# Performance work log

Measured on AMD Instinct MI355X. Metric: run time of the kernel, lower is better.

Reference implementation:

```python
import jax, jax.numpy as jnp
import numpy as np
from jax import lax

D_MODEL = 1024
EXPAND = 2
D_INNER = EXPAND * D_MODEL  # 2048
D_STATE = 16
D_CONV = 4
DT_RANK = -(-D_INNER // 16)  # ceil(d_inner/16) = 128
BATCH, SEQLEN = 2, 1024
LN_EPS = 1e-5


def setup_inputs() -> dict:
    key = jax.random.key(0)
    ks = jax.random.split(key, 8)
    s = lambda n: 1.0 / np.sqrt(n)
    x = jax.random.normal(ks[0], (BATCH, SEQLEN, D_MODEL), jnp.float32)
    ln_gamma = jnp.ones((D_MODEL,), jnp.float32)
    ln_beta = jnp.zeros((D_MODEL,), jnp.float32)
    in_proj_w = jax.random.normal(ks[1], (D_MODEL, 2 * D_INNER), jnp.float32) * s(D_MODEL)
    conv_w = jax.random.normal(ks[2], (D_INNER, D_CONV), jnp.float32) * s(D_CONV)
    conv_b = jnp.zeros((D_INNER,), jnp.float32)
    x_proj_w = jax.random.normal(ks[3], (D_INNER, DT_RANK + 2 * D_STATE), jnp.float32) * s(D_INNER)
    dt_proj_w = jax.random.uniform(ks[4], (DT_RANK, D_INNER), jnp.float32,
                                   -DT_RANK ** -0.5, DT_RANK ** -0.5)
    # dt bias init: inverse-softplus of dt ~ LogUniform(1e-3, 1e-1)
    dt = jnp.exp(jax.random.uniform(ks[5], (D_INNER,), jnp.float32)
                 * (np.log(0.1) - np.log(0.001)) + np.log(0.001))
    dt = jnp.clip(dt, 1e-4)
    dt_proj_b = dt + jnp.log(-jnp.expm1(-dt))
    A_log = jnp.log(jnp.tile(jnp.arange(1, D_STATE + 1, dtype=jnp.float32)[None, :],
                             (D_INNER, 1)))  # (D_INNER, D_STATE)
    D_param = jnp.ones((D_INNER,), jnp.float32)
    out_proj_w = jax.random.normal(ks[6], (D_INNER, D_MODEL), jnp.float32) * s(D_INNER)
    return {"x": x, "ln_gamma": ln_gamma, "ln_beta": ln_beta, "in_proj_w": in_proj_w,
            "conv_w": conv_w, "conv_b": conv_b, "x_proj_w": x_proj_w,
            "dt_proj_w": dt_proj_w, "dt_proj_b": dt_proj_b, "A_log": A_log,
            "D_param": D_param, "out_proj_w": out_proj_w}


def _layernorm(x, gamma, beta):
    mu = jnp.mean(x, -1, keepdims=True)
    var = jnp.mean(jnp.square(x - mu), -1, keepdims=True)
    return (x - mu) * lax.rsqrt(var + LN_EPS) * gamma + beta


def reference(x, ln_gamma, ln_beta, in_proj_w, conv_w, conv_b, x_proj_w,
              dt_proj_w, dt_proj_b, A_log, D_param, out_proj_w):
    B, L, _ = x.shape
    residual = x
    h = _layernorm(x, ln_gamma, ln_beta)
    xz = h @ in_proj_w                               # (B, L, 2*Di)
    xb, z = jnp.split(xz, 2, axis=-1)                # each (B, L, Di)

    # Depthwise causal conv1d (left pad d_conv-1, truncate to L)
    xp = jnp.pad(xb, ((0, 0), (D_CONV - 1, 0), (0, 0)))
    xc = sum(xp[:, k:k + L, :] * conv_w[:, k] for k in range(D_CONV)) + conv_b
    xb = jax.nn.silu(xc)                             # (B, L, Di)

    # Selective SSM
    xpj = xb @ x_proj_w                              # (B, L, dt_rank + 2N)
    dt_r = xpj[..., :DT_RANK]
    B_mat = xpj[..., DT_RANK:DT_RANK + D_STATE]      # (B, L, N)
    C_mat = xpj[..., DT_RANK + D_STATE:]             # (B, L, N)
    delta = jax.nn.softplus(dt_r @ dt_proj_w + dt_proj_b)  # (B, L, Di)
    A = -jnp.exp(A_log)                              # (Di, N)
    dA = jnp.exp(delta[..., None] * A)               # (B, L, Di, N)
    dBx = delta[..., None] * B_mat[:, :, None, :] * xb[..., None]  # (B, L, Di, N)

    def step(hcar, inp):
        dA_t, dBx_t, C_t = inp                       # (B,Di,N),(B,Di,N),(B,N)
        hcar = dA_t * hcar + dBx_t
        y_t = jnp.einsum('bdn,bn->bd', hcar, C_t)
        return hcar, y_t

    h0 = jnp.zeros((B, D_INNER, D_STATE), xb.dtype)
    _, ys = lax.scan(step, h0, (dA.transpose(1, 0, 2, 3),
                                dBx.transpose(1, 0, 2, 3),
                                C_mat.transpose(1, 0, 2)))
    y = ys.transpose(1, 0, 2) + xb * D_param         # (B, L, Di)

    y = y * jax.nn.silu(z)
    return y @ out_proj_w + residual
```

## Files before the change

### kernel.cpp

```cpp
#include <hip/hip_runtime.h>
#include <hip/hip_bf16.h>

#define D_MODEL 1024
#define D_INNER 2048
#define NPROJ   4096
#define D_STATE 16
#define DT_RANK 128
#define XPJ_N   160
#define SEQLEN  1024
#define BATCH   2
#define NTOK    2048
#define CHUNK   16
#define NCHUNK  (SEQLEN / CHUNK)
#define LOG2_NCHUNK 6
#define SPLITK  8
#define OP_SPLITK 4

typedef short short8 __attribute__((ext_vector_type(8)));
typedef unsigned short ushort8v __attribute__((ext_vector_type(8)));
typedef float f32x4 __attribute__((ext_vector_type(4)));

__device__ __forceinline__ float sigmoidf_(float x) { return 1.f / (1.f + __expf(-x)); }
__device__ __forceinline__ ushort f2bf_bits(float f) {
    __hip_bfloat16 h = __float2bfloat16(f);
    return *(ushort*)&h;
}
__device__ __forceinline__ float bf2f(ushort u) {
    union { unsigned int i; float f; } v;
    v.i = ((unsigned int)u) << 16;
    return v.f;
}
#define LOG2E 1.44269504088896f

__device__ __forceinline__ void transpose_tile(const float* __restrict__ in,
                                               ushort* __restrict__ out,
                                               int R, int C, int cx, int ry)
{
    __shared__ float tile[64][65];
    int c0 = cx * 64, r0 = ry * 64;
    #pragma unroll
    for (int i = 0; i < 16; ++i) {
        int idx = threadIdx.x + i * 256;
        int r = idx >> 6, c = idx & 63;
        tile[r][c] = (r0 + r < R && c0 + c < C) ? in[(long)(r0 + r) * C + (c0 + c)] : 0.f;
    }
    __syncthreads();
    #pragma unroll
    for (int i = 0; i < 16; ++i) {
        int idx = threadIdx.x + i * 256;
        int cc = idx >> 6, rr = idx & 63;
        if (c0 + cc < C && r0 + rr < R)
            out[(long)(c0 + cc) * R + (r0 + rr)] = f2bf_bits(tile[rr][cc]);
    }
}

__device__ __forceinline__ void ln_row(const float* __restrict__ x,
                                       const float* __restrict__ g,
                                       const float* __restrict__ be,
                                       ushort* __restrict__ hb, int row)
{
    __shared__ float red[8];
    const float4* xr = (const float4*)(x + (long)row * D_MODEL);
    float4 v = xr[threadIdx.x];
    float s1 = v.x + v.y + v.z + v.w;
    float s2 = v.x*v.x + v.y*v.y + v.z*v.z + v.w*v.w;
    for (int off = 32; off >= 1; off >>= 1) {
        s1 += __shfl_down(s1, off);
        s2 += __shfl_down(s2, off);
    }
    int wid = threadIdx.x >> 6;
    if ((threadIdx.x & 63) == 0) { red[wid] = s1; red[4 + wid] = s2; }
    __syncthreads();
    float mu  = (red[0] + red[1] + red[2] + red[3]) * (1.f / D_MODEL);
    float ex2 = (red[4] + red[5] + red[6] + red[7]) * (1.f / D_MODEL);
    float inv = rsqrtf(ex2 - mu * mu + 1e-5f);
    float4 g4 = ((const float4*)g)[threadIdx.x];
    float4 b4 = ((const float4*)be)[threadIdx.x];
    ushort4 o;
    o.x = f2bf_bits((v.x - mu) * inv * g4.x + b4.x);
    o.y = f2bf_bits((v.y - mu) * inv * g4.y + b4.y);
    o.z = f2bf_bits((v.z - mu) * inv * g4.z + b4.z);
    o.w = f2bf_bits((v.w - mu) * inv * g4.w + b4.w);
    *(ushort4*)(hb + (long)row * D_MODEL + threadIdx.x * 4) = o;
}

__global__ __launch_bounds__(256) void prep_kernel(const float* __restrict__ w2,
                                                   ushort* __restrict__ W2T,
                                                   const float* __restrict__ w7,
                                                   ushort* __restrict__ W7T,
                                                   const float* __restrict__ xp,
                                                   ushort* __restrict__ XPT,
                                                   const float* __restrict__ dt,
                                                   ushort* __restrict__ DTT,
                                                   const float* __restrict__ x,
                                                   const float* __restrict__ g,
                                                   const float* __restrict__ be,
                                                   ushort* __restrict__ hb)
{
    int idx = blockIdx.x;
    if (idx < 1024) {
        transpose_tile(w2, W2T, D_MODEL, NPROJ, idx & 63, idx >> 6);
    } else if (idx < 1536) {
        int rel = idx - 1024;
        transpose_tile(w7, W7T, D_INNER, D_MODEL, rel & 15, rel >> 4);
    } else if (idx < 1632) {
        int rel = idx - 1536;
        transpose_tile(xp, XPT, D_INNER, XPJ_N, rel % 3, rel / 3);
    } else if (idx < 1696) {
        int rel = idx - 1632;
        transpose_tile(dt, DTT, DT_RANK, D_INNER, rel & 31, rel >> 5);
    } else {
        ln_row(x, g, be, hb, idx - 1696);
    }
}

template <int EPI, int OBF>
__global__ __launch_bounds__(256) void gemm_mfma_kernel(const ushort* __restrict__ A,
                                                        const ushort* __restrict__ Bt,
                                                        const float* __restrict__ bias,
                                                        float* __restrict__ Cf,
                                                        ushort* __restrict__ Cb,
                                                        int M, int N, int K, int lda, int ldb)
{
    long zoff = (long)blockIdx.z;
    A  += zoff * K;
    Bt += zoff * K;
    if (OBF == 0) Cf += zoff * (long)M * N;
    else          Cb += zoff * (long)M * N;
    int lin = blockIdx.y * gridDim.x + blockIdx.x;
    int cpx = (gridDim.x * gridDim.y) >> 3;
    lin = (lin & 7) * cpx + (lin >> 3);
    int bx = lin % gridDim.x, by = lin / gridDim.x;
    __shared__ __align__(16) ushort Al[2][128 * 32];
    __shared__ __align__(16) ushort Bl[2][128 * 32];
    int tid = threadIdx.x;
    int lane = tid & 63;
    int w = tid >> 6, wr = w >> 1, wc = w & 1;
    int m0 = by * 128, n0 = bx * 128;
    f32x4 acc[4][4];
    #pragma unroll
    for (int m = 0; m < 4; ++m)
        #pragma unroll
        for (int n = 0; n < 4; ++n) acc[m][n] = (f32x4){0.f, 0.f, 0.f, 0.f};
    int l15 = lane & 15, kq = lane >> 4;

    auto stage = [&](int buf, int k0) {
        #pragma unroll
        for (int i = 0; i < 2; ++i) {
            int s = i * 256 + tid;
            int row = s >> 2, kg = s & 3;
            int kgl = kg ^ ((row >> 1) & 3);
            __builtin_amdgcn_global_load_lds(
                (const __attribute__((address_space(1))) void*)(A + (long)(m0 + row) * lda + k0 + kgl * 8),
                (__attribute__((address_space(3))) void*)(Al[buf] + s * 8), 16, 0, 0);
            __builtin_amdgcn_global_load_lds(
                (const __attribute__((address_space(1))) void*)(Bt + (long)(n0 + row) * ldb + k0 + kgl * 8),
                (__attribute__((address_space(3))) void*)(Bl[buf] + s * 8), 16, 0, 0);
        }
    };

    stage(0, 0);
    int cur = 0;
    for (int k0 = 0; k0 < K; k0 += 32) {
        if (k0 + 32 < K) {
            stage(cur ^ 1, k0 + 32);
            asm volatile("s_waitcnt vmcnt(4)" ::: "memory");
        } else {
            asm volatile("s_waitcnt vmcnt(0)" ::: "memory");
        }
        __builtin_amdgcn_s_barrier();
        asm volatile("" ::: "memory");
        short8 af[4], bf[4];
        #pragma unroll
        for (int m = 0; m < 4; ++m) {
            int row = wr * 64 + m * 16 + l15;
            af[m] = *(const short8*)&Al[cur][row * 32 + (kq ^ ((row >> 1) & 3)) * 8];
        }
        #pragma unroll
        for (int n = 0; n < 4; ++n) {
            int row = wc * 64 + n * 16 + l15;
            bf[n] = *(const short8*)&Bl[cur][row * 32 + (kq ^ ((row >> 1) & 3)) * 8];
        }
        __builtin_amdgcn_s_setprio(1);
        #pragma unroll
        for (int m = 0; m < 4; ++m)
            #pragma unroll
            for (int n = 0; n < 4; ++n)
                acc[m][n] = __builtin_amdgcn_mfma_f32_16x16x32_bf16(af[m], bf[n], acc[m][n], 0, 0, 0);
        __builtin_amdgcn_s_setprio(0);
        asm volatile("" ::: "memory");
        __builtin_amdgcn_s_barrier();
        asm volatile("" ::: "memory");
        cur ^= 1;
    }
    #pragma unroll
    for (int m = 0; m < 4; ++m) {
        #pragma unroll
        for (int n = 0; n < 4; ++n) {
            #pragma unroll
            for (int r = 0; r < 4; ++r) {
                int row = m0 + wr * 64 + m * 16 + kq * 4 + r;
                int col = n0 + wc * 64 + n * 16 + l15;
                float v = acc[m][n][r];
                if (EPI == 1) {
                    v += bias[col];
                    v = (v > 20.f) ? v : log1pf(__expf(v));
                }
                if (OBF) Cb[(long)row * N + col] = f2bf_bits(v);
                else     Cf[(long)row * N + col] = v;
            }
        }
    }
}

template <int EPI, int OBF>
__global__ __launch_bounds__(256) void gemm_mfma64_kernel(const ushort* __restrict__ A,
                                                          const ushort* __restrict__ Bt,
                                                          const float* __restrict__ bias,
                                                          float* __restrict__ Cf,
                                                          ushort* __restrict__ Cb,
                                                          int M, int N, int K)
{
    int lin = blockIdx.y * gridDim.x + blockIdx.x;
    int cpx = (gridDim.x * gridDim.y) >> 3;
    lin = (lin & 7) * cpx + (lin >> 3);
    int bx = lin % gridDim.x, by = lin / gridDim.x;
    __shared__ __align__(16) ushort Al[2][128 * 32];
    __shared__ __align__(16) ushort Bl[2][64 * 32];
    int tid = threadIdx.x;
    int lane = tid & 63;
    int w = tid >> 6, wr = w >> 1, wc = w & 1;
    int m0 = by * 128, n0 = bx * 64;
    f32x4 acc[4][2];
    #pragma unroll
    for (int m = 0; m < 4; ++m)
        #pragma unroll
        for (int n = 0; n < 2; ++n) acc[m][n] = (f32x4){0.f, 0.f, 0.f, 0.f};
    int l15 = lane & 15, kq = lane >> 4;

    auto stage = [&](int buf, int k0) {
        #pragma unroll
        for (int i = 0; i < 2; ++i) {
            int s = i * 256 + tid;
            int row = s >> 2, kg = s & 3;
            int kgl = kg ^ ((row >> 1) & 3);
            __builtin_amdgcn_global_load_lds(
                (const __attribute__((address_space(1))) void*)(A + (long)(m0 + row) * K + k0 + kgl * 8),
                (__attribute__((address_space(3))) void*)(Al[buf] + s * 8), 16, 0, 0);
        }
        {
            int s = tid;
            int row = s >> 2, kg = s & 3;
            int kgl = kg ^ ((row >> 1) & 3);
            __builtin_amdgcn_global_load_lds(
                (const __attribute__((address_space(1))) void*)(Bt + (long)(n0 + row) * K + k0 + kgl * 8),
                (__attribute__((address_space(3))) void*)(Bl[buf] + s * 8), 16, 0, 0);
        }
    };

    stage(0, 0);
    int cur = 0;
    for (int k0 = 0; k0 < K; k0 += 32) {
        if (k0 + 32 < K) {
            stage(cur ^ 1, k0 + 32);
            asm volatile("s_waitcnt vmcnt(3)" ::: "memory");
        } else {
            asm volatile("s_waitcnt vmcnt(0)" ::: "memory");
        }
        __builtin_amdgcn_s_barrier();
        asm volatile("" ::: "memory");
        short8 af[4], bf[2];
        #pragma unroll
        for (int m = 0; m < 4; ++m) {
            int row = wr * 64 + m * 16 + l15;
            af[m] = *(const short8*)&Al[cur][row * 32 + (kq ^ ((row >> 1) & 3)) * 8];
        }
        #pragma unroll
        for (int n = 0; n < 2; ++n) {
            int row = wc * 32 + n * 16 + l15;
            bf[n] = *(const short8*)&Bl[cur][row * 32 + (kq ^ ((row >> 1) & 3)) * 8];
        }
        __builtin_amdgcn_s_setprio(1);
        #pragma unroll
        for (int m = 0; m < 4; ++m)
            #pragma unroll
            for (int n = 0; n < 2; ++n)
                acc[m][n] = __builtin_amdgcn_mfma_f32_16x16x32_bf16(af[m], bf[n], acc[m][n], 0, 0, 0);
        __builtin_amdgcn_s_setprio(0);
        asm volatile("" ::: "memory");
        __builtin_amdgcn_s_barrier();
        asm volatile("" ::: "memory");
        cur ^= 1;
    }
    #pragma unroll
    for (int m = 0; m < 4; ++m) {
        #pragma unroll
        for (int n = 0; n < 2; ++n) {
            #pragma unroll
            for (int r = 0; r < 4; ++r) {
                int row = m0 + wr * 64 + m * 16 + kq * 4 + r;
                int col = n0 + wc * 32 + n * 16 + l15;
                float v = acc[m][n][r];
                if (EPI == 1) {
                    v += bias[col];
                    v = (v > 20.f) ? v : log1pf(__expf(v));
                }
                if (OBF) Cb[(long)row * N + col] = f2bf_bits(v);
                else     Cf[(long)row * N + col] = v;
            }
        }
    }
}

__global__ __launch_bounds__(256) void reduce_out_kernel(const ushort* __restrict__ Ppart,
                                                         const float* __restrict__ resid,
                                                         float* __restrict__ out)
{
    long i = (long)blockIdx.x * 256 + threadIdx.x;
    const long STRIDE = (long)NTOK * D_MODEL;
    float4 s;
    ushort4 p0 = ((const ushort4*)Ppart)[i];
    s.x = bf2f(p0.x); s.y = bf2f(p0.y); s.z = bf2f(p0.z); s.w = bf2f(p0.w);
    #pragma unroll
    for (int k = 1; k < OP_SPLITK; ++k) {
        ushort4 pk = ((const ushort4*)(Ppart + k * STRIDE))[i];
        s.x += bf2f(pk.x); s.y += bf2f(pk.y); s.z += bf2f(pk.z); s.w += bf2f(pk.w);
    }
    float4 r = ((const float4*)resid)[i];
    s.x += r.x; s.y += r.y; s.z += r.z; s.w += r.w;
    ((float4*)out)[i] = s;
}

__global__ __launch_bounds__(256) void gemm4_mfma_kernel(const ushort* __restrict__ A,
                                                         const ushort* __restrict__ Bt,
                                                         ushort* __restrict__ Ppart,
                                                         int M, int K)
{
    __shared__ __align__(16) ushort Al[64 * 32];
    __shared__ __align__(16) ushort Bl[160 * 32];
    int tid = threadIdx.x;
    int lane = tid & 63;
    int w = tid >> 6, wr = w >> 1, wc = w & 1;
    int sk = blockIdx.x;
    int m0 = blockIdx.y * 64;
    int kbase = sk * (K / SPLITK);
    f32x4 acc[2][5];
    #pragma unroll
    for (int m = 0; m < 2; ++m)
        #pragma unroll
        for (int n = 0; n < 5; ++n) acc[m][n] = (f32x4){0.f, 0.f, 0.f, 0.f};
    int l15 = lane & 15, kq = lane >> 4;

    for (int ks = 0; ks < K / SPLITK; ks += 32) {
        int k0 = kbase + ks;
        {
            int s = tid;
            int row = s >> 2, kg = s & 3;
            int kgl = kg ^ ((row >> 1) & 3);
            __builtin_amdgcn_global_load_lds(
                (const __attribute__((address_space(1))) void*)(A + (long)(m0 + row) * K + k0 + kgl * 8),
                (__attribute__((address_space(3))) void*)(Al + s * 8), 16, 0, 0);
        }
        #pragma unroll
        for (int i = 0; i < 3; ++i) {
            int s = i * 256 + tid;
            if (s < 640) {
                int row = s >> 2, kg = s & 3;
                int kgl = kg ^ ((row >> 1) & 3);
                __builtin_amdgcn_global_load_lds(
                    (const __attribute__((address_space(1))) void*)(Bt + (long)row * K + k0 + kgl * 8),
                    (__attribute__((address_space(3))) void*)(Bl + s * 8), 16, 0, 0);
            }
        }
        __syncthreads();
        short8 af[2], bf[5];
        #pragma unroll
        for (int m = 0; m < 2; ++m) {
            int row = wr * 32 + m * 16 + l15;
            af[m] = *(const short8*)&Al[row * 32 + (kq ^ ((row >> 1) & 3)) * 8];
        }
        #pragma unroll
        for (int n = 0; n < 5; ++n) {
            int row = wc * 80 + n * 16 + l15;
            bf[n] = *(const short8*)&Bl[row * 32 + (kq ^ ((row >> 1) & 3)) * 8];
        }
        #pragma unroll
        for (int m = 0; m < 2; ++m)
            #pragma unroll
            for (int n = 0; n < 5; ++n)
                acc[m][n] = __builtin_amdgcn_mfma_f32_16x16x32_bf16(af[m], bf[n], acc[m][n], 0, 0, 0);
        __syncthreads();
    }
    ushort* P = Ppart + (long)sk * M * XPJ_N;
    #pragma unroll
    for (int m = 0; m < 2; ++m) {
        #pragma unroll
        for (int n = 0; n < 5; ++n) {
            #pragma unroll
            for (int r = 0; r < 4; ++r) {
                int row = m0 + wr * 32 + m * 16 + kq * 4 + r;
                int col = wc * 80 + n * 16 + l15;
                P[(long)row * XPJ_N + col] = f2bf_bits(acc[m][n][r]);
            }
        }
    }
}

__global__ __launch_bounds__(256) void reduce_xpj_kernel(const ushort* __restrict__ Ppart,
                                                         float* __restrict__ xpj,
                                                         ushort* __restrict__ dtr)
{
    long i = (long)blockIdx.x * 256 + threadIdx.x;
    float s = 0.f;
    #pragma unroll
    for (int k = 0; k < SPLITK; ++k) s += bf2f(Ppart[k * (long)NTOK * XPJ_N + i]);
    xpj[i] = s;
    int col = (int)(i % XPJ_N);
    long row = i / XPJ_N;
    if (col < DT_RANK) dtr[row * DT_RANK + col] = f2bf_bits(s);
}

__global__ __launch_bounds__(256) void conv_silu_kernel(const ushort* __restrict__ xzb,
                                                        const float* __restrict__ cw,
                                                        const float* __restrict__ cb,
                                                        ushort* __restrict__ xbb)
{
    long i = (long)blockIdx.x * 256 + threadIdx.x;
    int d8 = (int)(i & (D_INNER / 8 - 1));
    long tok = i >> 8;
    int l = (int)(tok & (SEQLEN - 1));
    int d0 = d8 * 8;
    const ushort* base = xzb + tok * NPROJ + d0;
    ushort8v r3 = *(const ushort8v*)base;
    ushort8v r2 = {0,0,0,0,0,0,0,0}, r1 = r2, r0 = r2;
    if (l >= 1) r2 = *(const ushort8v*)(base - NPROJ);
    if (l >= 2) r1 = *(const ushort8v*)(base - 2 * NPROJ);
    if (l >= 3) r0 = *(const ushort8v*)(base - 3 * NPROJ);
    ushort8v o;
    #pragma unroll
    for (int j = 0; j < 8; ++j) {
        int d = d0 + j;
        float4 wv = *(const float4*)&cw[d * 4];
        float acc = cb[d]
                  + bf2f(r0[j]) * wv.x + bf2f(r1[j]) * wv.y
                  + bf2f(r2[j]) * wv.z + bf2f(r3[j]) * wv.w;
        o[j] = f2bf_bits(acc * sigmoidf_(acc));
    }
    *(ushort8v*)(xbb + tok * D_INNER + d0) = o;
}

__global__ __launch_bounds__(256) void scan_partial_kernel(const ushort* __restrict__ deltab,
                                                           const ushort* __restrict__ xbb,
                                                           const float* __restrict__ xpj,
                                                           const float* __restrict__ A_log,
                                                           ushort* __restrict__ Pout,
                                                           ushort* __restrict__ Hout)
{
    __shared__ float bc[CHUNK][16];
    int blk = blockIdx.x;
    int db = blk & 7;
    int c  = (blk >> 3) & (NCHUNK - 1);
    int b  = blk >> (3 + LOG2_NCHUNK);
    int d  = db * 256 + threadIdx.x;
    long tok0 = (long)b * SEQLEN + c * CHUNK;
    {
        int t = threadIdx.x >> 4, cc = threadIdx.x & 15;
        bc[t][cc] = xpj[(tok0 + t) * XPJ_N + DT_RANK + cc];
    }
    float a[16], h[16];
    #pragma unroll
    for (int q = 0; q < 4; ++q) {
        float4 al = *(const float4*)&A_log[d * D_STATE + q * 4];
        a[q*4+0] = -__expf(al.x) * LOG2E;
        a[q*4+1] = -__expf(al.y) * LOG2E;
        a[q*4+2] = -__expf(al.z) * LOG2E;
        a[q*4+3] = -__expf(al.w) * LOG2E;
    }
    #pragma unroll
    for (int n = 0; n < 16; ++n) h[n] = 0.f;
    float cum = 0.f;
    const ushort* dp = deltab + tok0 * D_INNER + d;
    const ushort* xp = xbb + tok0 * D_INNER + d;
    __syncthreads();
    #pragma unroll
    for (int t = 0; t < CHUNK; ++t) {
        float dl = bf2f(dp[(long)t * D_INNER]);
        float x  = bf2f(xp[(long)t * D_INNER]);
        float ux = dl * x;
        cum += dl;
        #pragma unroll
        for (int q = 0; q < 4; ++q) {
            float4 Bv = *(const float4*)&bc[t][q * 4];
            h[q*4+0] = exp2f(dl * a[q*4+0]) * h[q*4+0] + ux * Bv.x;
            h[q*4+1] = exp2f(dl * a[q*4+1]) * h[q*4+1] + ux * Bv.y;
            h[q*4+2] = exp2f(dl * a[q*4+2]) * h[q*4+2] + ux * Bv.z;
            h[q*4+3] = exp2f(dl * a[q*4+3]) * h[q*4+3] + ux * Bv.w;
        }
    }
    long chbase = ((long)(b * NCHUNK + c) * D_INNER + d) * D_STATE;
    #pragma unroll
    for (int q = 0; q < 4; ++q) {
        ushort4 pv;
        pv.x = f2bf_bits(exp2f(a[q*4+0] * cum));
        pv.y = f2bf_bits(exp2f(a[q*4+1] * cum));
        pv.z = f2bf_bits(exp2f(a[q*4+2] * cum));
        pv.w = f2bf_bits(exp2f(a[q*4+3] * cum));
        *(ushort4*)&Pout[chbase + q * 4] = pv;
        ushort4 hv;
        hv.x = f2bf_bits(h[q*4+0]); hv.y = f2bf_bits(h[q*4+1]);
        hv.z = f2bf_bits(h[q*4+2]); hv.w = f2bf_bits(h[q*4+3]);
        *(ushort4*)&Hout[chbase + q * 4] = hv;
    }
}

__global__ __launch_bounds__(256) void scan_chunkscan_kernel(const ushort* __restrict__ P,
                                                             const ushort* __restrict__ H,
                                                             ushort* __restrict__ hinit)
{
    long i = (long)blockIdx.x * 256 + threadIdx.x;
    int n = (int)(i & (D_STATE - 1));
    int d = (int)((i >> 4) & (D_INNER - 1));
    int b = (int)(i >> 15);
    const long cstride = (long)D_INNER * D_STATE;
    long base = ((long)b * NCHUNK) * cstride + (long)d * D_STATE + n;
    float h = 0.f;
    for (int g = 0; g < NCHUNK / 8; ++g) {
        ushort Pr[8], Hr[8];
        #pragma unroll
        for (int j = 0; j < 8; ++j) {
            long o = base + (long)(g * 8 + j) * cstride;
            Pr[j] = P[o];
            Hr[j] = H[o];
        }
        #pragma unroll
        for (int j = 0; j < 8; ++j) {
            long o = base + (long)(g * 8 + j) * cstride;
            hinit[o] = f2bf_bits(h);
            h = bf2f(Pr[j]) * h + bf2f(Hr[j]);
        }
    }
}

__global__ __launch_bounds__(256) void scan_final_kernel(const ushort* __restrict__ deltab,
                                                         const ushort* __restrict__ xbb,
                                                         const float* __restrict__ xpj,
                                                         const ushort* __restrict__ xzb,
                                                         const float* __restrict__ A_log,
                                                         const float* __restrict__ Dp,
                                                         const ushort* __restrict__ hinit,
                                                         ushort* __restrict__ yb)
{
    __shared__ float bc[CHUNK][32];
    int blk = blockIdx.x;
    int db = blk & 7;
    int c  = (blk >> 3) & (NCHUNK - 1);
    int b  = blk >> (3 + LOG2_NCHUNK);
    int d  = db * 256 + threadIdx.x;
    long tok0 = (long)b * SEQLEN + c * CHUNK;
    for (int i = threadIdx.x; i < CHUNK * 32; i += 256) {
        int t = i >> 5, cc = i & 31;
        bc[t][cc] = xpj[(tok0 + t) * XPJ_N + DT_RANK + cc];
    }
    float a[16], h[16];
    #pragma unroll
    for (int q = 0; q < 4; ++q) {
        float4 al = *(const float4*)&A_log[d * D_STATE + q * 4];
        a[q*4+0] = -__expf(al.x) * LOG2E;
        a[q*4+1] = -__expf(al.y) * LOG2E;
        a[q*4+2] = -__expf(al.z) * LOG2E;
        a[q*4+3] = -__expf(al.w) * LOG2E;
    }
    long chbase = ((long)(b * NCHUNK + c) * D_INNER + d) * D_STATE;
    #pragma unroll
    for (int q = 0; q < 4; ++q) {
        ushort4 hv = *(const ushort4*)&hinit[chbase + q * 4];
        h[q*4+0] = bf2f(hv.x); h[q*4+1] = bf2f(hv.y);
        h[q*4+2] = bf2f(hv.z); h[q*4+3] = bf2f(hv.w);
    }
    float dpar = Dp[d];
    const ushort* dp = deltab + tok0 * D_INNER + d;
    const ushort* xp = xbb + tok0 * D_INNER + d;
    const ushort* zp = xzb + tok0 * NPROJ + D_INNER + d;
    ushort* yp = yb + tok0 * D_INNER + d;
    __syncthreads();
    #pragma unroll
    for (int t = 0; t < CHUNK; ++t) {
        float dl = bf2f(dp[(long)t * D_INNER]);
        float x  = bf2f(xp[(long)t * D_INNER]);
        float z  = bf2f(zp[(long)t * NPROJ]);
        float ux = dl * x;
        float y = 0.f;
        #pragma unroll
        for (int q = 0; q < 4; ++q) {
            float4 Bv = *(const float4*)&bc[t][q * 4];
            float4 Cv = *(const float4*)&bc[t][16 + q * 4];
            h[q*4+0] = exp2f(dl * a[q*4+0]) * h[q*4+0] + ux * Bv.x;
            h[q*4+1] = exp2f(dl * a[q*4+1]) * h[q*4+1] + ux * Bv.y;
            h[q*4+2] = exp2f(dl * a[q*4+2]) * h[q*4+2] + ux * Bv.z;
            h[q*4+3] = exp2f(dl * a[q*4+3]) * h[q*4+3] + ux * Bv.w;
            y += h[q*4+0] * Cv.x + h[q*4+1] * Cv.y + h[q*4+2] * Cv.z + h[q*4+3] * Cv.w;
        }
        y += x * dpar;
        yp[(long)t * D_INNER] = f2bf_bits(y * (z * sigmoidf_(z)));
    }
}

extern "C" void kernel_launch(void* const* d_in, const int* in_sizes, int n_in,
                              void* d_out, int out_size, void* d_ws, size_t ws_size,
                              hipStream_t stream) {
    const float* x         = (const float*)d_in[0];
    const float* ln_gamma  = (const float*)d_in[1];
    const float* ln_beta   = (const float*)d_in[2];
    const float* in_proj_w = (const float*)d_in[3];
    const float* conv_w    = (const float*)d_in[4];
    const float* conv_b    = (const float*)d_in[5];
    const float* x_proj_w  = (const float*)d_in[6];
    const float* dt_proj_w = (const float*)d_in[7];
    const float* dt_proj_b = (const float*)d_in[8];
    const float* A_log     = (const float*)d_in[9];
    const float* D_param   = (const float*)d_in[10];
    const float* out_proj_w= (const float*)d_in[11];
    float* out = (float*)d_out;

    float* p = (float*)d_ws;
    ushort* hb      = (ushort*)p; p += 1048576;
    ushort* W2T     = (ushort*)p; p += 2097152;
    ushort* W7T     = (ushort*)p; p += 1048576;
    ushort* XPT     = (ushort*)p; p += 163840;
    ushort* DTT     = (ushort*)p; p += 131072;
    ushort* xz_bf16 = (ushort*)p; p += 4194304;
    ushort* xb_bf16 = (ushort*)p; p += 2097152;
    float*  xpj     = p;          p += 327680;
    ushort* dtr     = (ushort*)p; p += 131072;
    ushort* delta_bf16 = (ushort*)p; p += 2097152;
    ushort* Ppart   = (ushort*)p; p += 1310720;
    ushort* Pbuf    = (ushort*)p; p += 2097152;
    ushort* Hbuf    = (ushort*)p; p += 2097152;
    ushort* hinit   = (ushort*)p; p += 2097152;
    ushort* y_bf16  = (ushort*)p; p += 2097152;
    ushort* PpartO  = (ushort*)p; p += 4194304;

    prep_kernel<<<1696 + NTOK, 256, 0, stream>>>(
        in_proj_w, W2T, out_proj_w, W7T, x_proj_w, XPT, dt_proj_w, DTT,
        x, ln_gamma, ln_beta, hb);

    gemm_mfma_kernel<0, 1><<<dim3(NPROJ / 128, NTOK / 128), 256, 0, stream>>>(
        hb, W2T, nullptr, nullptr, xz_bf16, NTOK, NPROJ, D_MODEL, D_MODEL, D_MODEL);

    conv_silu_kernel<<<(NTOK * D_INNER / 8) / 256, 256, 0, stream>>>(
        xz_bf16, conv_w, conv_b, xb_bf16);

    gemm4_mfma_kernel<<<dim3(SPLITK, NTOK / 64), 256, 0, stream>>>(
        xb_bf16, XPT, Ppart, NTOK, D_INNER);
    reduce_xpj_kernel<<<(NTOK * XPJ_N) / 256, 256, 0, stream>>>(Ppart, xpj, dtr);

    gemm_mfma64_kernel<1, 1><<<dim3(D_INNER / 64, NTOK / 128), 256, 0, stream>>>(
        dtr, DTT, dt_proj_b, nullptr, delta_bf16, NTOK, D_INNER, DT_RANK);

    scan_partial_kernel<<<BATCH * NCHUNK * 8, 256, 0, stream>>>(
        delta_bf16, xb_bf16, xpj, A_log, Pbuf, Hbuf);
    scan_chunkscan_kernel<<<(BATCH * D_INNER * D_STATE) / 256, 256, 0, stream>>>(
        Pbuf, Hbuf, hinit);
    scan_final_kernel<<<BATCH * NCHUNK * 8, 256, 0, stream>>>(
        delta_bf16, xb_bf16, xpj, xz_bf16, A_log, D_param, hinit, y_bf16);

    gemm_mfma_kernel<0, 1><<<dim3(D_MODEL / 128, NTOK / 128, OP_SPLITK), 256, 0, stream>>>(
        y_bf16, W7T, nullptr, nullptr, PpartO, NTOK, D_MODEL, D_INNER / OP_SPLITK,
        D_INNER, D_INNER);
    reduce_out_kernel<<<(NTOK * D_MODEL / 4) / 256, 256, 0, stream>>>(PpartO, x, out);
}
```

Measured before the change: 166.3 us.

## Replace split-K out-projection with 64x64-tile GEMM fusing residual add

The out-projection previously ran a 128x128-tile GEMM split four ways over K, writing bf16 partials that a separate kernel reduced and added to the residual. A new 64x64-tile MFMA kernel now covers the full K and adds the residual in its epilogue. This removes the partial-buffer traffic and one launch, and uses smaller tiles to keep 512 blocks. The x_proj split-K factor is also raised from 8 to 16, with its partial buffer enlarged to match. The cost is lower per-block data reuse from the small tiles, a longer serial K loop, and more partial sums to reduce for x_proj.

```diff
diff --git a/kernel.cpp b/kernel.cpp
--- a/kernel.cpp
+++ b/kernel.cpp
@@ -13,8 +13,7 @@
 #define CHUNK   16
 #define NCHUNK  (SEQLEN / CHUNK)
 #define LOG2_NCHUNK 6
-#define SPLITK  8
-#define OP_SPLITK 4
+#define SPLITK  16
 
 typedef short short8 __attribute__((ext_vector_type(8)));
 typedef unsigned short ushort8v __attribute__((ext_vector_type(8)));
@@ -122,11 +121,6 @@
                                                         ushort* __restrict__ Cb,
                                                         int M, int N, int K, int lda, int ldb)
 {
-    long zoff = (long)blockIdx.z;
-    A  += zoff * K;
-    Bt += zoff * K;
-    if (OBF == 0) Cf += zoff * (long)M * N;
-    else          Cb += zoff * (long)M * N;
     int lin = blockIdx.y * gridDim.x + blockIdx.x;
     int cpx = (gridDim.x * gridDim.y) >> 3;
     lin = (lin & 7) * cpx + (lin >> 3);
@@ -312,23 +306,87 @@
     }
 }
 
-__global__ __launch_bounds__(256) void reduce_out_kernel(const ushort* __restrict__ Ppart,
-                                                         const float* __restrict__ resid,
-                                                         float* __restrict__ out)
-{
-    long i = (long)blockIdx.x * 256 + threadIdx.x;
-    const long STRIDE = (long)NTOK * D_MODEL;
-    float4 s;
-    ushort4 p0 = ((const ushort4*)Ppart)[i];
-    s.x = bf2f(p0.x); s.y = bf2f(p0.y); s.z = bf2f(p0.z); s.w = bf2f(p0.w);
-    #pragma unroll
-    for (int k = 1; k < OP_SPLITK; ++k) {
-        ushort4 pk = ((const ushort4*)(Ppart + k * STRIDE))[i];
-        s.x += bf2f(pk.x); s.y += bf2f(pk.y); s.z += bf2f(pk.z); s.w += bf2f(pk.w);
-    }
-    float4 r = ((const float4*)resid)[i];
-    s.x += r.x; s.y += r.y; s.z += r.z; s.w += r.w;
-    ((float4*)out)[i] = s;
+__global__ __launch_bounds__(256) void gemm_op64_kernel(const ushort* __restrict__ A,
+                                                        const ushort* __restrict__ Bt,
+                                                        const float* __restrict__ resid,
+                                                        float* __restrict__ out,
+                                                        int M, int N, int K)
+{
+    int lin = blockIdx.y * gridDim.x + blockIdx.x;
+    int cpx = (gridDim.x * gridDim.y) >> 3;
+    lin = (lin & 7) * cpx + (lin >> 3);
+    int bx = lin % gridDim.x, by = lin / gridDim.x;
+    __shared__ __align__(16) ushort Al[2][64 * 32];
+    __shared__ __align__(16) ushort Bl[2][64 * 32];
+    int tid = threadIdx.x;
+    int lane = tid & 63;
+    int w = tid >> 6, wr = w >> 1, wc = w & 1;
+    int m0 = by * 64, n0 = bx * 64;
+    f32x4 acc[2][2];
+    #pragma unroll
+    for (int m = 0; m < 2; ++m)
+        #pragma unroll
+        for (int n = 0; n < 2; ++n) acc[m][n] = (f32x4){0.f, 0.f, 0.f, 0.f};
+    int l15 = lane & 15, kq = lane >> 4;
+
+    auto stage = [&](int buf, int k0) {
+        int s = tid;
+        int row = s >> 2, kg = s & 3;
+        int kgl = kg ^ ((row >> 1) & 3);
+        __builtin_amdgcn_global_load_lds(
+            (const __attribute__((address_space(1))) void*)(A + (long)(m0 + row) * K + k0 + kgl * 8),
+            (__attribute__((address_space(3))) void*)(Al[buf] + s * 8), 16, 0, 0);
+        __builtin_amdgcn_global_load_lds(
+            (const __attribute__((address_space(1))) void*)(Bt + (long)(n0 + row) * K + k0 + kgl * 8),
+            (__attribute__((address_space(3))) void*)(Bl[buf] + s * 8), 16, 0, 0);
+    };
+
+    stage(0, 0);
+    int cur = 0;
+    for (int k0 = 0; k0 < K; k0 += 32) {
+        if (k0 + 32 < K) {
+            stage(cur ^ 1, k0 + 32);
+            asm volatile("s_waitcnt vmcnt(2)" ::: "memory");
+        } else {
+            asm volatile("s_waitcnt vmcnt(0)" ::: "memory");
+        }
+        __builtin_amdgcn_s_barrier();
+        asm volatile("" ::: "memory");
+        short8 af[2], bf[2];
+        #pragma unroll
+        for (int m = 0; m < 2; ++m) {
+            int row = wr * 32 + m * 16 + l15;
+            af[m] = *(const short8*)&Al[cur][row * 32 + (kq ^ ((row >> 1) & 3)) * 8];
+        }
+        #pragma unroll
+        for (int n = 0; n < 2; ++n) {
+            int row = wc * 32 + n * 16 + l15;
+            bf[n] = *(const short8*)&Bl[cur][row * 32 + (kq ^ ((row >> 1) & 3)) * 8];
+        }
+        __builtin_amdgcn_s_setprio(1);
+        #pragma unroll
+        for (int m = 0; m < 2; ++m)
+            #pragma unroll
+            for (int n = 0; n < 2; ++n)
+                acc[m][n] = __builtin_amdgcn_mfma_f32_16x16x32_bf16(af[m], bf[n], acc[m][n], 0, 0, 0);
+        __builtin_amdgcn_s_setprio(0);
+        asm volatile("" ::: "memory");
+        __builtin_amdgcn_s_barrier();
+        asm volatile("" ::: "memory");
+        cur ^= 1;
+    }
+    #pragma unroll
+    for (int m = 0; m < 2; ++m) {
+        #pragma unroll
+        for (int n = 0; n < 2; ++n) {
+            #pragma unroll
+            for (int r = 0; r < 4; ++r) {
+                int row = m0 + wr * 32 + m * 16 + kq * 4 + r;
+                int col = n0 + wc * 32 + n * 16 + l15;
+                out[(long)row * N + col] = acc[m][n][r] + resid[(long)row * N + col];
+            }
+        }
+    }
 }
 
 __global__ __launch_bounds__(256) void gemm4_mfma_kernel(const ushort* __restrict__ A,
@@ -633,12 +691,11 @@
     float*  xpj     = p;          p += 327680;
     ushort* dtr     = (ushort*)p; p += 131072;
     ushort* delta_bf16 = (ushort*)p; p += 2097152;
-    ushort* Ppart   = (ushort*)p; p += 1310720;
+    ushort* Ppart   = (ushort*)p; p += 2621440;
     ushort* Pbuf    = (ushort*)p; p += 2097152;
     ushort* Hbuf    = (ushort*)p; p += 2097152;
     ushort* hinit   = (ushort*)p; p += 2097152;
     ushort* y_bf16  = (ushort*)p; p += 2097152;
-    ushort* PpartO  = (ushort*)p; p += 4194304;
 
     prep_kernel<<<1696 + NTOK, 256, 0, stream>>>(
         in_proj_w, W2T, out_proj_w, W7T, x_proj_w, XPT, dt_proj_w, DTT,
@@ -664,8 +721,6 @@
     scan_final_kernel<<<BATCH * NCHUNK * 8, 256, 0, stream>>>(
         delta_bf16, xb_bf16, xpj, xz_bf16, A_log, D_param, hinit, y_bf16);
 
-    gemm_mfma_kernel<0, 1><<<dim3(D_MODEL / 128, NTOK / 128, OP_SPLITK), 256, 0, stream>>>(
-        y_bf16, W7T, nullptr, nullptr, PpartO, NTOK, D_MODEL, D_INNER / OP_SPLITK,
-        D_INNER, D_INNER);
-    reduce_out_kernel<<<(NTOK * D_MODEL / 4) / 256, 256, 0, stream>>>(PpartO, x, out);
-}
+    gemm_op64_kernel<<<dim3(D_MODEL / 64, NTOK / 64), 256, 0, stream>>>(
+        y_bf16, W7T, x, out, NTOK, D_MODEL, D_INNER);
+}
```

Measured after the change: 170.8 us. +2.7%, slower.
